# Performance work log

Measured on AMD Instinct MI355X. Metric: run time of the kernel, lower is better.

## Reference

```python
import jax, jax.numpy as jnp
import numpy as np

HEAD_SIZE = 64
N_EMBD = 1024
B, T = 8, 4096

def setup_inputs() -> dict:
    key = jax.random.key(0)
    k1, k2, k3, k4 = jax.random.split(key, 4)
    x = jax.random.normal(k1, (B, T, N_EMBD), dtype=jnp.float32)
    # bias-free Linear weights, stored as [in, out] so y = x @ W
    scale = 1.0 / np.sqrt(N_EMBD)
    Wk = jax.random.uniform(k2, (N_EMBD, HEAD_SIZE), jnp.float32, -scale, scale)
    Wq = jax.random.uniform(k3, (N_EMBD, HEAD_SIZE), jnp.float32, -scale, scale)
    Wv = jax.random.uniform(k4, (N_EMBD, HEAD_SIZE), jnp.float32, -scale, scale)
    return {"x": x, "Wk": Wk, "Wq": Wq, "Wv": Wv}

def reference(x, Wk, Wq, Wv):
    # x: [B, T, C]
    k = x @ Wk  # [B, T, H]
    q = x @ Wq
    v = x @ Wv
    scale = HEAD_SIZE ** -0.5
    wei = jnp.einsum('bth,bsh->bts', q, k) * scale  # [B, T, T]
    Tn = x.shape[1]
    causal = jnp.tril(jnp.ones((Tn, Tn), dtype=bool))
    wei = jnp.where(causal, wei, -jnp.inf)
    wei = jax.nn.softmax(wei, axis=-1)
    # dropout p=0.0 -> identity (eval behavior)
    out = jnp.einsum('bts,bsh->bth', wei, v)  # [B, T, H]
    return out
```

## Files before the change

kernel.cpp:

```cpp
#include <hip/hip_runtime.h>
#include <hip/hip_bf16.h>


#define HS 64
#define NE 1024
#define NB 8
#define TS 4096
#define NROW (NB * TS)

#define QKV_BUF 20480
#define QKV_XB  12288

typedef __attribute__((ext_vector_type(4)))  float f32x4;
typedef __attribute__((ext_vector_type(16))) float f32x16;
typedef __attribute__((ext_vector_type(8)))  short s16x8;
typedef __attribute__((ext_vector_type(4)))  float vfloat4;

__device__ __forceinline__ unsigned short f2bf(float x) {
  return __builtin_bit_cast(unsigned short, __float2bfloat16(x));
}
__device__ __forceinline__ unsigned pkbf(float lo, float hi) {
  return (unsigned)f2bf(lo) | ((unsigned)f2bf(hi) << 16);
}
__device__ __forceinline__ unsigned cvtpk(float lo, float hi) {
  unsigned r;
  asm("v_cvt_pk_bf16_f32 %0, %1, %2" : "=v"(r) : "v"(lo), "v"(hi));
  return r;
}

union ABFrag { s16x8 v; unsigned d[4]; };

__device__ __forceinline__ void gl_lds16(const void* g, const unsigned char* l) {
  __builtin_amdgcn_global_load_lds(
      (const __attribute__((address_space(1))) unsigned int*)(g),
      (__attribute__((address_space(3))) unsigned int*)(l), 16, 0, 0);
}

__global__ __launch_bounds__(256) void wt_kernel(const float* __restrict__ Wk,
                                                 const float* __restrict__ Wq,
                                                 const float* __restrict__ Wv,
                                                 unsigned short* __restrict__ wT2) {
  __shared__ float lds[3 * 2048];
  const int c = blockIdx.x;
  const int t = threadIdx.x;
  const int base = c * 2048;
  const float4* wq4 = (const float4*)(Wq + base);
  const float4* wk4 = (const float4*)(Wk + base);
  const float4* wv4 = (const float4*)(Wv + base);
  float4* l4 = (float4*)lds;
  l4[t]              = wq4[t];
  l4[t + 256]        = wq4[t + 256];
  l4[512 + t]        = wk4[t];
  l4[512 + t + 256]  = wk4[t + 256];
  l4[1024 + t]       = wv4[t];
  l4[1024 + t + 256] = wv4[t + 256];
  __syncthreads();
#pragma unroll
  for (int u = 0; u < 24; ++u) {
    const int o = t + 256 * u;
    const int j = o & 7, sk = o >> 3;
    const int g = sk / 192, n = sk % 192;
    const int m = n >> 6, col = n & 63;
    float v = lds[m * 2048 + (g * 8 + j) * 64 + col];
    if (m == 0) v *= 0.18033688011112042f;
    wT2[(size_t)c * 6144 + o] = f2bf(v);
  }
}

__global__ __launch_bounds__(256, 4) void qkv_kernel(const float* __restrict__ x,
                                                     const unsigned short* __restrict__ wT2,
                                                     unsigned short* __restrict__ q_ws,
                                                     unsigned short* __restrict__ kf,
                                                     unsigned short* __restrict__ vf) {
  __shared__ __align__(16) unsigned char smem[2 * QKV_BUF];
  const int t = threadIdx.x;
  const int w = t >> 6, lane = t & 63;
  const int g = lane >> 4, nn = lane & 15;
  const int m0blk = blockIdx.x * 64;
  const int m0 = m0blk + w * 16;

  f32x4 acc[12];
#pragma unroll
  for (int i = 0; i < 12; ++i) acc[i] = f32x4{0.f, 0.f, 0.f, 0.f};

  const unsigned short* wsrcA = wT2 + (size_t)(w * 192 + lane) * 8;
  const int wd0 = w * 3072;
  const float* xs0 = x + (size_t)(m0blk + w * 16 + 0 + (lane >> 3)) * NE + (lane & 7) * 4;
  const float* xs1 = x + (size_t)(m0blk + w * 16 + 8 + (lane >> 3)) * NE + (lane & 7) * 4;
  const int xd0 = QKV_XB + w * 2048;
  const int xd1 = xd0 + 1024;

  const int abase = QKV_XB + (w * 16 + nn) * 128 + g * 32;
  const int wbase = (g * 192 + nn) * 16;

#define ISSUE(C)                                                               \
  {                                                                            \
    unsigned char* db_ = smem + ((C) & 1) * QKV_BUF;                           \
    gl_lds16(wsrcA + (size_t)(C) * 6144, db_ + wd0);                           \
    gl_lds16(wsrcA + (size_t)(C) * 6144 + 512, db_ + wd0 + 1024);              \
    gl_lds16(wsrcA + (size_t)(C) * 6144 + 1024, db_ + wd0 + 2048);             \
    gl_lds16(xs0 + (C) * 32, db_ + xd0);                                       \
    gl_lds16(xs1 + (C) * 32, db_ + xd1);                                       \
  }

  ISSUE(0)
  __builtin_amdgcn_sched_barrier(0);
  ISSUE(1)
  __builtin_amdgcn_sched_barrier(0);

#define PHASE(C, VM, DOISS)                                                    \
  {                                                                            \
    asm volatile("s_waitcnt vmcnt(" #VM ")" ::: "memory");                     \
    __builtin_amdgcn_s_barrier();                                              \
    __builtin_amdgcn_sched_barrier(0);                                         \
    const unsigned char* bb_ = smem + ((C) & 1) * QKV_BUF;                     \
    const vfloat4 a0_ = *(const vfloat4*)(bb_ + abase);                        \
    const vfloat4 a1_ = *(const vfloat4*)(bb_ + abase + 16);                   \
    ABFrag af;                                                                 \
    af.d[0] = pkbf(a0_.x, a0_.y); af.d[1] = pkbf(a0_.z, a0_.w);                \
    af.d[2] = pkbf(a1_.x, a1_.y); af.d[3] = pkbf(a1_.z, a1_.w);                \
    _Pragma("unroll")                                                          \
    for (int i = 0; i < 12; ++i) {                                             \
      const s16x8 bf = *(const s16x8*)(bb_ + wbase + i * 256);                 \
      acc[i] = __builtin_amdgcn_mfma_f32_16x16x32_bf16(af.v, bf, acc[i], 0, 0, 0); \
    }                                                                          \
    __builtin_amdgcn_sched_barrier(0);                                         \
    __builtin_amdgcn_s_barrier();                                              \
    __builtin_amdgcn_sched_barrier(0);                                         \
    if (DOISS) { ISSUE((C) + 2) }                                              \
    __builtin_amdgcn_sched_barrier(0);                                         \
  }

#pragma unroll
  for (int c = 0; c < 30; ++c) PHASE(c, 5, 1)
  PHASE(30, 5, 0)
  PHASE(31, 0, 0)
#undef PHASE
#undef ISSUE

  __syncthreads();
  unsigned short* kfs = (unsigned short*)smem;
  unsigned short* vfs = kfs + 4096;
  const int rbase = m0 + 4 * g;
#pragma unroll
  for (int i = 0; i < 12; ++i) {
    const int c = 16 * i + nn;
#pragma unroll
    for (int j = 0; j < 4; ++j) {
      const int rr = rbase + j;
      const unsigned short hval = f2bf(acc[i][j]);
      if (c < 64) {
        q_ws[(size_t)rr * HS + c] = hval;
      } else {
        const int r5 = rr & 31;
        const int sbl = (rr >> 5) & 1;
        if (c < 128) {
          const int h = c - 64;
          kfs[sbl * 2048 + (h >> 4) * 512 + ((h >> 3) & 1) * 256 + r5 * 8 + (h & 7)] = hval;
        } else {
          const int h = c - 128;
          vfs[sbl * 2048 + (h >> 5) * 1024 + ((r5 >> 4) & 1) * 512 +
              ((r5 >> 3) & 1) * 256 + (h & 31) * 8 + (r5 & 7)] = hval;
        }
      }
    }
  }
  __syncthreads();
  {
    const int bb0 = m0blk >> 12;
    const int sb0 = (m0blk & 4095) >> 5;
    const uint4* ks = (const uint4*)kfs;
    const uint4* vs = (const uint4*)vfs;
    uint4* kd = (uint4*)(kf + (size_t)bb0 * 262144 + (size_t)sb0 * 2048);
    uint4* vd = (uint4*)(vf + (size_t)bb0 * 262144 + (size_t)sb0 * 2048);
#pragma unroll
    for (int u = 0; u < 2; ++u) {
      kd[t + u * 256] = ks[t + u * 256];
      vd[t + u * 256] = vs[t + u * 256];
    }
  }
}

#define TILE32F(DIAG, KF, VF, QF, L_RUN, O)                                    \
  {                                                                            \
    f32x16 st_;                                                                \
    __builtin_amdgcn_s_setprio(1);                                             \
    st_ = __builtin_amdgcn_mfma_f32_32x32x16_bf16(KF[0], QF[0], zz, 0, 0, 0);  \
    st_ = __builtin_amdgcn_mfma_f32_32x32x16_bf16(KF[1], QF[1], st_, 0, 0, 0); \
    st_ = __builtin_amdgcn_mfma_f32_32x32x16_bf16(KF[2], QF[2], st_, 0, 0, 0); \
    st_ = __builtin_amdgcn_mfma_f32_32x32x16_bf16(KF[3], QF[3], st_, 0, 0, 0); \
    __builtin_amdgcn_s_setprio(0);                                             \
    if (DIAG) {                                                                \
      _Pragma("unroll") for (int r = 0; r < 16; ++r) {                         \
        const int kvl_ = (r & 3) + 8 * (r >> 2) + hi4;                         \
        if (kvl_ > qi) st_[r] = -1e30f;                                        \
      }                                                                        \
    }                                                                          \
    float p_[16];                                                              \
    _Pragma("unroll") for (int r = 0; r < 16; ++r)                             \
      p_[r] = __builtin_amdgcn_exp2f(st_[r]);                                  \
    float sm_ = ((p_[0] + p_[1]) + (p_[2] + p_[3])) +                          \
                ((p_[4] + p_[5]) + (p_[6] + p_[7]));                           \
    sm_ += ((p_[8] + p_[9]) + (p_[10] + p_[11])) +                             \
           ((p_[12] + p_[13]) + (p_[14] + p_[15]));                            \
    L_RUN += sm_;                                                              \
    const unsigned q01_ = cvtpk(p_[0], p_[1]),   q23_ = cvtpk(p_[2], p_[3]);   \
    const unsigned q45_ = cvtpk(p_[4], p_[5]),   q67_ = cvtpk(p_[6], p_[7]);   \
    const unsigned q89_ = cvtpk(p_[8], p_[9]),   qab_ = cvtpk(p_[10], p_[11]); \
    const unsigned qcd_ = cvtpk(p_[12], p_[13]), qef_ = cvtpk(p_[14], p_[15]); \
    const unsigned e0_ = (unsigned)__shfl_xor((int)(hi ? q01_ : q45_), 32, 64);\
    const unsigned e1_ = (unsigned)__shfl_xor((int)(hi ? q23_ : q67_), 32, 64);\
    const unsigned e2_ = (unsigned)__shfl_xor((int)(hi ? q89_ : qcd_), 32, 64);\
    const unsigned e3_ = (unsigned)__shfl_xor((int)(hi ? qab_ : qef_), 32, 64);\
    ABFrag pf0_, pf1_;                                                         \
    pf0_.d[0] = hi ? e0_ : q01_;                                               \
    pf0_.d[1] = hi ? e1_ : q23_;                                               \
    pf0_.d[2] = hi ? q45_ : e0_;                                               \
    pf0_.d[3] = hi ? q67_ : e1_;                                               \
    pf1_.d[0] = hi ? e2_ : q89_;                                               \
    pf1_.d[1] = hi ? e3_ : qab_;                                               \
    pf1_.d[2] = hi ? qcd_ : e2_;                                               \
    pf1_.d[3] = hi ? qef_ : e3_;                                               \
    __builtin_amdgcn_s_setprio(1);                                             \
    O[0] = __builtin_amdgcn_mfma_f32_32x32x16_bf16(VF[0], pf0_.v, O[0], 0,0,0);\
    O[0] = __builtin_amdgcn_mfma_f32_32x32x16_bf16(VF[1], pf1_.v, O[0], 0,0,0);\
    O[1] = __builtin_amdgcn_mfma_f32_32x32x16_bf16(VF[2], pf0_.v, O[1], 0,0,0);\
    O[1] = __builtin_amdgcn_mfma_f32_32x32x16_bf16(VF[3], pf1_.v, O[1], 0,0,0);\
    __builtin_amdgcn_s_setprio(0);                                             \
  }

#define LD4(dst, base)                                                         \
  dst[0] = *(const s16x8*)(base);                                              \
  dst[1] = *(const s16x8*)((base) + 512);                                      \
  dst[2] = *(const s16x8*)((base) + 1024);                                     \
  dst[3] = *(const s16x8*)((base) + 1536);

__global__ __launch_bounds__(512, 4) void attn_kernel(const unsigned short* __restrict__ q_ws,
                                                      const unsigned short* __restrict__ kf,
                                                      const unsigned short* __restrict__ vf,
                                                      float* __restrict__ out) {
  __shared__ float o_sm[2][4][16][68];
  __shared__ float l_sm[2][4][32];

  const int wv = threadIdx.x >> 6, lane = threadIdx.x & 63;
  const int qi = lane & 31, hi = lane >> 5;
  const int hi8 = 8 * hi, hi4 = 4 * hi;

  const int bid = blockIdx.x;
  const int b = bid & 7;
  const int pr = bid >> 3;
  const int tile = wv >> 2;
  const int wq = wv & 3;
  const int ti_x = tile ? (127 - pr) : pr;
  const int t0 = ti_x * 32;

  const unsigned short* kfb = kf + (size_t)b * 262144 + lane * 8;
  const unsigned short* vfb = vf + (size_t)b * 262144 + lane * 8;
  const unsigned short* qr = q_ws + (size_t)(b * TS + t0 + qi) * HS + hi8;

  s16x8 qf[4];
#pragma unroll
  for (int kk = 0; kk < 4; ++kk) qf[kk] = *(const s16x8*)(qr + 16 * kk);

  f32x16 o[2];
#pragma unroll
  for (int r = 0; r < 16; ++r) { o[0][r] = 0.f; o[1][r] = 0.f; }
  float l_run = 0.f;

  f32x16 zz;
#pragma unroll
  for (int r = 0; r < 16; ++r) zz[r] = 0.f;

  for (int it = wq; it < ti_x; it += 4) {
    s16x8 kfr[4], vfr[4];
    LD4(kfr, kfb + (size_t)it * 2048)
    LD4(vfr, vfb + (size_t)it * 2048)
    TILE32F(0, kfr, vfr, qf, l_run, o)
  }
  if ((ti_x & 3) == wq) {
    s16x8 kfr[4], vfr[4];
    LD4(kfr, kfb + (size_t)ti_x * 2048)
    LD4(vfr, vfb + (size_t)ti_x * 2048)
    TILE32F(1, kfr, vfr, qf, l_run, o)
  }

  l_run += __shfl_xor(l_run, 32, 64);

  if (lane < 32) l_sm[tile][wq][lane] = l_run;
  const int X = threadIdx.x >> 8;
  const int rem = threadIdx.x & 255;
  const int q8m = rem >> 4;
  const int h0 = (rem & 15) * 4;
  const int t0X = (X ? (127 - pr) : pr) * 32;

#pragma unroll
  for (int P = 0; P < 2; ++P) {
    if ((qi >> 4) == P) {
      const int qr_ = qi & 15;
#pragma unroll
      for (int ht = 0; ht < 2; ++ht)
#pragma unroll
        for (int r = 0; r < 16; ++r) {
          const int h = ht * 32 + (r & 3) + 8 * (r >> 2) + hi4;
          o_sm[tile][wq][qr_][h] = o[ht][r];
        }
    }
    __syncthreads();
    {
      const int q = 16 * P + q8m;
      const float L = l_sm[X][0][q] + l_sm[X][1][q] +
                      l_sm[X][2][q] + l_sm[X][3][q];
      const float inv = 1.0f / L;
      float rv[4];
#pragma unroll
      for (int j = 0; j < 4; ++j)
        rv[j] = (o_sm[X][0][q8m][h0 + j] + o_sm[X][1][q8m][h0 + j] +
                 o_sm[X][2][q8m][h0 + j] + o_sm[X][3][q8m][h0 + j]) * inv;
      *(float4*)(out + ((size_t)(b * TS + t0X + q)) * HS + h0) =
          float4{rv[0], rv[1], rv[2], rv[3]};
    }
    if (P == 0) __syncthreads();
  }
}

extern "C" void kernel_launch(void* const* d_in, const int* in_sizes, int n_in,
                              void* d_out, int out_size, void* d_ws, size_t ws_size,
                              hipStream_t stream) {
  const float* x  = (const float*)d_in[0];
  const float* Wk = (const float*)d_in[1];
  const float* Wq = (const float*)d_in[2];
  const float* Wv = (const float*)d_in[3];
  float* out = (float*)d_out;

  unsigned short* wT2  = (unsigned short*)d_ws;
  unsigned short* q_ws = wT2 + 192 * 1024;
  unsigned short* kf   = q_ws + (size_t)NROW * HS;
  unsigned short* vf   = kf + (size_t)NROW * HS;

  wt_kernel<<<dim3(32), dim3(256), 0, stream>>>(Wk, Wq, Wv, wT2);
  qkv_kernel<<<dim3(NROW / 64), dim3(256), 0, stream>>>(x, wT2, q_ws, kf, vf);
  attn_kernel<<<dim3(512), dim3(512), 0, stream>>>(q_ws, kf, vf, out);
}
```

Before: 58.66 us.

## Stage K/V tiles in double-buffered LDS shared by two adjacent query tiles

The attention kernel now gives each block two adjacent 32-row query tiles instead of a balanced pair of short and long tiles. Each iteration cooperatively loads 128 keys of K and V from global memory directly into LDS with async gl_lds16 copies, double-buffered so the next chunk loads while the current one is computed. K/V traffic is shared across the 8 waves, which removes redundant per-wave global loads and overlaps memory with MFMA work. In exchange it needs 64KB of LDS, adds two block barriers per iteration, and drops the pairing that balanced causal work across blocks, so per-block work now varies with position.

```diff
diff --git a/kernel.cpp b/kernel.cpp
--- a/kernel.cpp
+++ b/kernel.cpp
@@ -229,34 +229,29 @@
     __builtin_amdgcn_s_setprio(0);                                             \
   }
 
-#define LD4(dst, base)                                                         \
-  dst[0] = *(const s16x8*)(base);                                              \
-  dst[1] = *(const s16x8*)((base) + 512);                                      \
-  dst[2] = *(const s16x8*)((base) + 1024);                                     \
-  dst[3] = *(const s16x8*)((base) + 1536);
-
 __global__ __launch_bounds__(512, 4) void attn_kernel(const unsigned short* __restrict__ q_ws,
                                                       const unsigned short* __restrict__ kf,
                                                       const unsigned short* __restrict__ vf,
                                                       float* __restrict__ out) {
-  __shared__ float o_sm[2][4][16][68];
+  __shared__ __align__(16) unsigned char smem[65536];
   __shared__ float l_sm[2][4][32];
 
-  const int wv = threadIdx.x >> 6, lane = threadIdx.x & 63;
+  const int t = threadIdx.x;
+  const int wv = t >> 6, lane = t & 63;
   const int qi = lane & 31, hi = lane >> 5;
   const int hi8 = 8 * hi, hi4 = 4 * hi;
 
   const int bid = blockIdx.x;
   const int b = bid & 7;
-  const int pr = bid >> 3;
-  const int tile = wv >> 2;
-  const int wq = wv & 3;
-  const int ti_x = tile ? (127 - pr) : pr;
-  const int t0 = ti_x * 32;
-
-  const unsigned short* kfb = kf + (size_t)b * 262144 + lane * 8;
-  const unsigned short* vfb = vf + (size_t)b * 262144 + lane * 8;
-  const unsigned short* qr = q_ws + (size_t)(b * TS + t0 + qi) * HS + hi8;
+  const int p = bid >> 3;
+  const int sub = wv >> 2, wq = wv & 3;
+  const int tqs = 2 * p + sub;
+  const int jmax = (2 * p + 2 + 3) >> 2;
+  const int t0w = p * 64 + sub * 32;
+
+  const unsigned short* kfb = kf + (size_t)b * 262144;
+  const unsigned short* vfb = vf + (size_t)b * 262144;
+  const unsigned short* qr = q_ws + (size_t)(b * TS + t0w + qi) * HS + hi8;
 
   s16x8 qf[4];
 #pragma unroll
@@ -266,32 +261,57 @@
 #pragma unroll
   for (int r = 0; r < 16; ++r) { o[0][r] = 0.f; o[1][r] = 0.f; }
   float l_run = 0.f;
-
   f32x16 zz;
 #pragma unroll
   for (int r = 0; r < 16; ++r) zz[r] = 0.f;
 
-  for (int it = wq; it < ti_x; it += 4) {
-    s16x8 kfr[4], vfr[4];
-    LD4(kfr, kfb + (size_t)it * 2048)
-    LD4(vfr, vfb + (size_t)it * 2048)
-    TILE32F(0, kfr, vfr, qf, l_run, o)
-  }
-  if ((ti_x & 3) == wq) {
-    s16x8 kfr[4], vfr[4];
-    LD4(kfr, kfb + (size_t)ti_x * 2048)
-    LD4(vfr, vfb + (size_t)ti_x * 2048)
-    TILE32F(1, kfr, vfr, qf, l_run, o)
+#define AISSUE(J)                                                              \
+  {                                                                            \
+    const int jc_ = ((J) < jmax) ? (J) : (jmax - 1);                           \
+    unsigned char* db_ = smem + ((J) & 1) * 32768;                             \
+    const unsigned short* ksrc_ = kfb + (size_t)jc_ * 8192 + t * 8;            \
+    const unsigned short* vsrc_ = vfb + (size_t)jc_ * 8192 + t * 8;            \
+    gl_lds16(ksrc_, db_ + t * 16);                                             \
+    gl_lds16(ksrc_ + 4096, db_ + 8192 + t * 16);                               \
+    gl_lds16(vsrc_, db_ + 16384 + t * 16);                                     \
+    gl_lds16(vsrc_ + 4096, db_ + 24576 + t * 16);                              \
+  }
+
+  AISSUE(0)
+  __builtin_amdgcn_sched_barrier(0);
+
+  for (int j = 0; j < jmax; ++j) {
+    AISSUE(j + 1)
+    asm volatile("s_waitcnt vmcnt(4)" ::: "memory");
+    __builtin_amdgcn_s_barrier();
+    __builtin_amdgcn_sched_barrier(0);
+    const int tg = 4 * j + wq;
+    if (tg <= tqs) {
+      const unsigned char* bb = smem + (j & 1) * 32768;
+      const unsigned char* kb = bb + wq * 4096 + lane * 16;
+      const unsigned char* vb = bb + 16384 + wq * 4096 + lane * 16;
+      s16x8 kfr[4], vfr[4];
+#pragma unroll
+      for (int i = 0; i < 4; ++i) {
+        kfr[i] = *(const s16x8*)(kb + i * 1024);
+        vfr[i] = *(const s16x8*)(vb + i * 1024);
+      }
+      TILE32F(tg == tqs, kfr, vfr, qf, l_run, o)
+    }
+    __builtin_amdgcn_sched_barrier(0);
+    __builtin_amdgcn_s_barrier();
+    __builtin_amdgcn_sched_barrier(0);
   }
 
   l_run += __shfl_xor(l_run, 32, 64);
 
-  if (lane < 32) l_sm[tile][wq][lane] = l_run;
-  const int X = threadIdx.x >> 8;
-  const int rem = threadIdx.x & 255;
+  float* o_sm = (float*)smem;
+  if (lane < 32) l_sm[sub][wq][lane] = l_run;
+  const int X = t >> 8;
+  const int rem = t & 255;
   const int q8m = rem >> 4;
   const int h0 = (rem & 15) * 4;
-  const int t0X = (X ? (127 - pr) : pr) * 32;
+  const int t0X = p * 64 + X * 32;
 
 #pragma unroll
   for (int P = 0; P < 2; ++P) {
@@ -302,7 +322,7 @@
 #pragma unroll
         for (int r = 0; r < 16; ++r) {
           const int h = ht * 32 + (r & 3) + 8 * (r >> 2) + hi4;
-          o_sm[tile][wq][qr_][h] = o[ht][r];
+          o_sm[((sub * 4 + wq) * 16 + qr_) * 68 + h] = o[ht][r];
         }
     }
     __syncthreads();
@@ -314,8 +334,10 @@
       float rv[4];
 #pragma unroll
       for (int j = 0; j < 4; ++j)
-        rv[j] = (o_sm[X][0][q8m][h0 + j] + o_sm[X][1][q8m][h0 + j] +
-                 o_sm[X][2][q8m][h0 + j] + o_sm[X][3][q8m][h0 + j]) * inv;
+        rv[j] = (o_sm[((X * 4 + 0) * 16 + q8m) * 68 + h0 + j] +
+                 o_sm[((X * 4 + 1) * 16 + q8m) * 68 + h0 + j] +
+                 o_sm[((X * 4 + 2) * 16 + q8m) * 68 + h0 + j] +
+                 o_sm[((X * 4 + 3) * 16 + q8m) * 68 + h0 + j]) * inv;
       *(float4*)(out + ((size_t)(b * TS + t0X + q)) * HS + h0) =
           float4{rv[0], rv[1], rv[2], rv[3]};
     }
```

Result: slower. 76.24 us (+30.0%).
